# Optimization experiments

Hardware: AMD Instinct MI355X
Metric: run time of the kernel (lower is better)

## Reference

```python
import jax, jax.numpy as jnp
import numpy as np

EMBED_DIM = 512
NUM_HEADS = 8
HEAD_DIM = EMBED_DIM // NUM_HEADS
SHIFT_INIT = 5.0
EPS = 1e-6


def setup_inputs() -> dict:
    key = jax.random.key(0)
    ks = jax.random.split(key, 8)
    L, N, E = 2048, 4, EMBED_DIM
    query = jax.random.normal(ks[0], (L, N, E), dtype=jnp.float32)
    k_in = jax.random.normal(ks[1], (L, N, E), dtype=jnp.float32)
    v_in = jax.random.normal(ks[2], (L, N, E), dtype=jnp.float32)
    # MultiheadAttention packed projections
    in_proj_weight = jax.random.normal(ks[3], (3 * E, E), dtype=jnp.float32) / np.sqrt(E)
    in_proj_bias = jnp.zeros((3 * E,), dtype=jnp.float32)
    out_proj_weight = jax.random.normal(ks[4], (E, E), dtype=jnp.float32) / np.sqrt(E)
    out_proj_bias = jnp.zeros((E,), dtype=jnp.float32)
    # GeM parameters: p ~ N(1, 0.02), shift = 5
    p = 1.0 + 0.02 * jax.random.normal(ks[5], (E,), dtype=jnp.float32)
    shift = jnp.full((E,), SHIFT_INIT, dtype=jnp.float32)
    return {
        "query": query, "key": k_in, "value": v_in,
        "in_proj_weight": in_proj_weight, "in_proj_bias": in_proj_bias,
        "out_proj_weight": out_proj_weight, "out_proj_bias": out_proj_bias,
        "p": p, "shift": shift,
    }


def reference(query, key, value, in_proj_weight, in_proj_bias,
              out_proj_weight, out_proj_bias, p, shift):
    L, N, E = query.shape
    H, D = NUM_HEADS, HEAD_DIM
    w_q, w_k, w_v = jnp.split(in_proj_weight, 3, axis=0)   # each (E, E)
    b_q, b_k, b_v = jnp.split(in_proj_bias, 3, axis=0)

    def proj(x, w, b):
        # (L, N, E) -> (N, H, L, D)
        y = x @ w.T + b
        return y.reshape(L, N, H, D).transpose(1, 2, 0, 3)

    q = proj(query, w_q, b_q)
    k = proj(key, w_k, b_k)
    v = proj(value, w_v, b_v)

    scale = 1.0 / np.sqrt(D)
    scores = jnp.einsum('nhld,nhsd->nhls', q, k) * scale   # (N,H,L,S)
    attn = jax.nn.softmax(scores, axis=-1)

    # GeM pooling of values: shift -> power p -> weighted mean -> inverse power -> unshift
    p_h = p.reshape(H, D)[None, :, None, :]                # (1,H,1,D)
    shift_h = shift.reshape(H, D)[None, :, None, :]
    v_pos = jnp.maximum(v + shift_h, EPS)                  # keep base positive
    pooled = jnp.einsum('nhls,nhsd->nhld', attn, v_pos ** p_h)
    out_h = jnp.maximum(pooled, EPS) ** (1.0 / p_h) - shift_h  # (N,H,L,D)

    out = out_h.transpose(2, 0, 1, 3).reshape(L, N, E)     # back to (L,N,E)
    out = out @ out_proj_weight.T + out_proj_bias
    return out
```

## Files before the change

### kernel.cpp

```cpp
#include <hip/hip_runtime.h>
#include <hip/hip_bf16.h>

#define E_DIM 512
#define N_BATCH 4
#define L_SEQ 2048
#define N_HEADS 8
#define H_DIM 64
#define N_ROWS (L_SEQ * N_BATCH)
#define EPS_F 1e-6f
#define SC_Q 0.18033688f

typedef __attribute__((ext_vector_type(8))) short bf16x8;
typedef __attribute__((ext_vector_type(8))) _Float16 f16x8;
typedef __attribute__((ext_vector_type(4))) float f32x4;
typedef __attribute__((ext_vector_type(16))) float f32x16;

__device__ __forceinline__ void split2(float f, __hip_bfloat16& h, __hip_bfloat16& l) {
  h = __float2bfloat16(f);
  l = __float2bfloat16(f - __bfloat162float(h));
}

__device__ __forceinline__ unsigned int packf16(float a, float b) {
  union { _Float16 h[2]; unsigned int u; } c;
  c.h[0] = (_Float16)a;
  c.h[1] = (_Float16)b;
  return c.u;
}

__global__ __launch_bounds__(256) void wconv_kernel(
    const float* __restrict__ wio, const float* __restrict__ wo,
    __hip_bfloat16* __restrict__ wiohi, __hip_bfloat16* __restrict__ wiolo,
    __hip_bfloat16* __restrict__ wohi, __hip_bfloat16* __restrict__ wolo) {
  const int g = blockIdx.x * 256 + threadIdx.x;
  const float* src;
  __hip_bfloat16 *dh, *dl;
  int i;
  if (g < 196608) { src = wio; dh = wiohi; dl = wiolo; i = g * 4; }
  else            { src = wo;  dh = wohi;  dl = wolo;  i = (g - 196608) * 4; }
  const float4 f = *(const float4*)(src + i);
  alignas(8) __hip_bfloat16 h[4], l[4];
  split2(f.x, h[0], l[0]); split2(f.y, h[1], l[1]);
  split2(f.z, h[2], l[2]); split2(f.w, h[3], l[3]);
  *(uint2*)(dh + i) = *(const uint2*)h;
  *(uint2*)(dl + i) = *(const uint2*)l;
}

__global__ __launch_bounds__(256, 3) void proj_qkv_kernel(
    const float* __restrict__ xq, const float* __restrict__ xk,
    const float* __restrict__ xv, const __hip_bfloat16* __restrict__ whi,
    const float* __restrict__ bias, const float* __restrict__ pw,
    const float* __restrict__ sw,
    _Float16* __restrict__ qbuf, _Float16* __restrict__ kbuf,
    float* __restrict__ ubuf) {
  __shared__ __hip_bfloat16 Xh[128][40];
  __shared__ __hip_bfloat16 Xl[128][40];
  __shared__ __hip_bfloat16 Wh[128][40];
  const int z = blockIdx.z;
  const int row0 = blockIdx.x * 128;
  const int col0 = blockIdx.y * 128;
  const float* __restrict__ xsrc = (z == 0) ? xq : (z == 1) ? xk : xv;
  const int tid = threadIdx.x;
  const int lane = tid & 63;
  const int wv = tid >> 6;
  const int lidx = lane & 15;
  const int quad = lane >> 4;
  const int srow = tid >> 1;
  const int scol = (tid & 1) * 16;

  f32x4 acc[2][8];
#pragma unroll
  for (int rt = 0; rt < 2; ++rt)
#pragma unroll
    for (int ct = 0; ct < 8; ++ct) acc[rt][ct] = (f32x4){0.f, 0.f, 0.f, 0.f};

  const int ar0 = wv * 32 + lidx;

  for (int kt = 0; kt < 16; ++kt) {
    const int k0 = kt * 32;
    {
      const float* xp = xsrc + (size_t)(row0 + srow) * E_DIM + k0 + scol;
      float f[16];
      *(float4*)&f[0]  = ((const float4*)xp)[0];
      *(float4*)&f[4]  = ((const float4*)xp)[1];
      *(float4*)&f[8]  = ((const float4*)xp)[2];
      *(float4*)&f[12] = ((const float4*)xp)[3];
      alignas(16) __hip_bfloat16 hi[16], lo[16];
#pragma unroll
      for (int j = 0; j < 16; ++j) split2(f[j], hi[j], lo[j]);
      *(uint4*)&Xh[srow][scol]     = ((const uint4*)hi)[0];
      *(uint4*)&Xh[srow][scol + 8] = ((const uint4*)hi)[1];
      *(uint4*)&Xl[srow][scol]     = ((const uint4*)lo)[0];
      *(uint4*)&Xl[srow][scol + 8] = ((const uint4*)lo)[1];
    }
    {
      const size_t wof = (size_t)(z * E_DIM + col0 + srow) * E_DIM + k0 + scol;
      *(uint4*)&Wh[srow][scol]     = ((const uint4*)(whi + wof))[0];
      *(uint4*)&Wh[srow][scol + 8] = ((const uint4*)(whi + wof))[1];
    }
    __syncthreads();

    const bf16x8 ah0 = *(const bf16x8*)&Xh[ar0][quad * 8];
    const bf16x8 ah1 = *(const bf16x8*)&Xh[ar0 + 16][quad * 8];
    const bf16x8 al0 = *(const bf16x8*)&Xl[ar0][quad * 8];
    const bf16x8 al1 = *(const bf16x8*)&Xl[ar0 + 16][quad * 8];
#pragma unroll
    for (int ct = 0; ct < 8; ++ct) {
      const bf16x8 bh = *(const bf16x8*)&Wh[ct * 16 + lidx][quad * 8];
      acc[0][ct] = __builtin_amdgcn_mfma_f32_16x16x32_bf16(ah0, bh, acc[0][ct], 0, 0, 0);
      acc[0][ct] = __builtin_amdgcn_mfma_f32_16x16x32_bf16(al0, bh, acc[0][ct], 0, 0, 0);
      acc[1][ct] = __builtin_amdgcn_mfma_f32_16x16x32_bf16(ah1, bh, acc[1][ct], 0, 0, 0);
      acc[1][ct] = __builtin_amdgcn_mfma_f32_16x16x32_bf16(al1, bh, acc[1][ct], 0, 0, 0);
    }
    __syncthreads();
  }

  if (z < 2) {
    _Float16* __restrict__ dst = (z == 0) ? qbuf : kbuf;
    const float scale = (z == 0) ? SC_Q : 1.0f;
    float bv[8];
#pragma unroll
    for (int ct = 0; ct < 8; ++ct) bv[ct] = bias[z * E_DIM + col0 + ct * 16 + lidx];
#pragma unroll
    for (int rt = 0; rt < 2; ++rt)
#pragma unroll
      for (int ct = 0; ct < 8; ++ct) {
        const int e = col0 + ct * 16 + lidx;
        const int h = e >> 6, d = e & 63;
#pragma unroll
        for (int reg = 0; reg < 4; ++reg) {
          const int R = row0 + wv * 32 + rt * 16 + quad * 4 + reg;
          const int lpos = R >> 2, nb = R & 3;
          dst[(((size_t)nb * N_HEADS + h) * L_SEQ + lpos) * H_DIM + d] =
              (_Float16)((acc[rt][ct][reg] + bv[ct]) * scale);
        }
      }
  } else {
    float bv[8], pv[8], sv[8];
#pragma unroll
    for (int ct = 0; ct < 8; ++ct) {
      const int e = col0 + ct * 16 + lidx;
      bv[ct] = bias[2 * E_DIM + e]; pv[ct] = pw[e]; sv[ct] = sw[e];
    }
#pragma unroll
    for (int rt = 0; rt < 2; ++rt)
#pragma unroll
      for (int ct = 0; ct < 8; ++ct) {
        const int e = col0 + ct * 16 + lidx;
        const int h = e >> 6, d = e & 63;
#pragma unroll
        for (int reg = 0; reg < 4; ++reg) {
          const int R = row0 + wv * 32 + rt * 16 + quad * 4 + reg;
          const int lpos = R >> 2, nb = R & 3;
          const float y = acc[rt][ct][reg] + bv[ct];
          const float vp = fmaxf(y + sv[ct], EPS_F);
          ubuf[(((size_t)nb * N_HEADS + h) * L_SEQ + lpos) * H_DIM + d] =
              __powf(vp, pv[ct]);
        }
      }
  }
}

__global__ __launch_bounds__(256) void transp_kernel(
    const float* __restrict__ u, _Float16* __restrict__ uT) {
  __shared__ float T[64][65];
  const int lt = blockIdx.x, h = blockIdx.y, nb = blockIdx.z;
  const int tid = threadIdx.x;
  const int r = tid >> 2;
  const int cb = (tid & 3) * 16;
  const size_t srcbase = ((size_t)nb * N_HEADS + h) * L_SEQ + lt * 64;
  {
    const float* p = u + (srcbase + r) * H_DIM + cb;
    *(float4*)&T[r][cb + 0]  = ((const float4*)p)[0];
    *(float4*)&T[r][cb + 4]  = ((const float4*)p)[1];
    *(float4*)&T[r][cb + 8]  = ((const float4*)p)[2];
    *(float4*)&T[r][cb + 12] = ((const float4*)p)[3];
  }
  __syncthreads();
  alignas(16) _Float16 hv[16];
#pragma unroll
  for (int j = 0; j < 16; ++j) hv[j] = (_Float16)T[cb + j][r];
  const size_t dst = (((size_t)nb * N_HEADS + h) * H_DIM + r) * L_SEQ + lt * 64 + cb;
  *(uint4*)(uT + dst)     = ((const uint4*)hv)[0];
  *(uint4*)(uT + dst + 8) = ((const uint4*)hv)[1];
}

__global__ __launch_bounds__(128, 2) void attn_kernel(
    const _Float16* __restrict__ qbuf, const _Float16* __restrict__ kbuf,
    const _Float16* __restrict__ uT, const float* __restrict__ pw,
    const float* __restrict__ sw, __hip_bfloat16* __restrict__ ohhi,
    __hip_bfloat16* __restrict__ ohlo) {
  __shared__ _Float16 Ks[64][72];
  __shared__ _Float16 Us[64][72];
  const int qt = blockIdx.x, h = blockIdx.y, nb = blockIdx.z;
  const int q0 = qt * 128;
  const int tid = threadIdx.x;
  const int lane = tid & 63;
  const int wv = tid >> 6;
  const int lm = lane & 31;
  const int kg = lane >> 5;
  const int srow = tid >> 1;
  const int scb = (tid & 1) * 32;
  const size_t headbase = ((size_t)nb * N_HEADS + h) * L_SEQ;
  const size_t dbase = ((size_t)nb * N_HEADS + h) * H_DIM;

  f16x8 bq[2][4];
#pragma unroll
  for (int nt = 0; nt < 2; ++nt)
#pragma unroll
    for (int kc = 0; kc < 4; ++kc)
      bq[nt][kc] = *(const f16x8*)(qbuf +
          (headbase + q0 + wv * 64 + nt * 32 + lm) * H_DIM + kc * 16 + kg * 8);

  f32x16 o[2][2];
  o[0][0] = (f32x16)(0.f); o[0][1] = (f32x16)(0.f);
  o[1][0] = (f32x16)(0.f); o[1][1] = (f32x16)(0.f);
  float lsum[2] = {0.f, 0.f};

  for (int scn = 0; scn < 32; ++scn) {
    const int s0 = scn * 64;
    __syncthreads();
    {
      const _Float16* kp = kbuf + (headbase + s0 + srow) * H_DIM + scb;
      *(uint4*)&Ks[srow][scb + 0]  = ((const uint4*)kp)[0];
      *(uint4*)&Ks[srow][scb + 8]  = ((const uint4*)kp)[1];
      *(uint4*)&Ks[srow][scb + 16] = ((const uint4*)kp)[2];
      *(uint4*)&Ks[srow][scb + 24] = ((const uint4*)kp)[3];
      const _Float16* up = uT + (dbase + srow) * L_SEQ + s0 + scb;
      *(uint4*)&Us[srow][scb + 0]  = ((const uint4*)up)[0];
      *(uint4*)&Us[srow][scb + 8]  = ((const uint4*)up)[1];
      *(uint4*)&Us[srow][scb + 16] = ((const uint4*)up)[2];
      *(uint4*)&Us[srow][scb + 24] = ((const uint4*)up)[3];
    }
    __syncthreads();

    f32x16 sc[2][2];
    sc[0][0] = (f32x16)(0.f); sc[0][1] = (f32x16)(0.f);
    sc[1][0] = (f32x16)(0.f); sc[1][1] = (f32x16)(0.f);
#pragma unroll
    for (int kc = 0; kc < 4; ++kc) {
      const f16x8 ak0 = *(const f16x8*)&Ks[lm][kc * 16 + kg * 8];
      const f16x8 ak1 = *(const f16x8*)&Ks[32 + lm][kc * 16 + kg * 8];
      sc[0][0] = __builtin_amdgcn_mfma_f32_32x32x16_f16(ak0, bq[0][kc], sc[0][0], 0, 0, 0);
      sc[0][1] = __builtin_amdgcn_mfma_f32_32x32x16_f16(ak1, bq[0][kc], sc[0][1], 0, 0, 0);
      sc[1][0] = __builtin_amdgcn_mfma_f32_32x32x16_f16(ak0, bq[1][kc], sc[1][0], 0, 0, 0);
      sc[1][1] = __builtin_amdgcn_mfma_f32_32x32x16_f16(ak1, bq[1][kc], sc[1][1], 0, 0, 0);
    }

    unsigned int P2[2][2][4][2];
#pragma unroll
    for (int nt = 0; nt < 2; ++nt)
#pragma unroll
      for (int mt = 0; mt < 2; ++mt)
#pragma unroll
        for (int g = 0; g < 4; ++g) {
          const float p0 = __builtin_amdgcn_exp2f(sc[nt][mt][4 * g + 0]);
          const float p1 = __builtin_amdgcn_exp2f(sc[nt][mt][4 * g + 1]);
          const float p2 = __builtin_amdgcn_exp2f(sc[nt][mt][4 * g + 2]);
          const float p3 = __builtin_amdgcn_exp2f(sc[nt][mt][4 * g + 3]);
          lsum[nt] += (p0 + p1) + (p2 + p3);
          P2[nt][mt][g][0] = packf16(p0, p1);
          P2[nt][mt][g][1] = packf16(p2, p3);
        }

#pragma unroll
    for (int kc = 0; kc < 4; ++kc) {
      const int mt = kc >> 1;
      const f16x8 au0 = *(const f16x8*)&Us[lm][kc * 16 + kg * 8];
      const f16x8 au1 = *(const f16x8*)&Us[32 + lm][kc * 16 + kg * 8];
#pragma unroll
      for (int nt = 0; nt < 2; ++nt) {
        const int gx = (2 * kc) & 3, gy = (2 * kc + 1) & 3;
        const unsigned int x0 = P2[nt][mt][gx][0], x1 = P2[nt][mt][gx][1];
        const unsigned int y0 = P2[nt][mt][gy][0], y1 = P2[nt][mt][gy][1];
        const unsigned int sA = kg ? x0 : y0, sB = kg ? x1 : y1;
        const unsigned int rA = (unsigned int)__shfl_xor((int)sA, 32);
        const unsigned int rB = (unsigned int)__shfl_xor((int)sB, 32);
        union { unsigned int u[4]; f16x8 v; } bp;
        bp.u[0] = kg ? rA : x0;
        bp.u[1] = kg ? rB : x1;
        bp.u[2] = kg ? y0 : rA;
        bp.u[3] = kg ? y1 : rB;
        o[nt][0] = __builtin_amdgcn_mfma_f32_32x32x16_f16(au0, bp.v, o[nt][0], 0, 0, 0);
        o[nt][1] = __builtin_amdgcn_mfma_f32_32x32x16_f16(au1, bp.v, o[nt][1], 0, 0, 0);
      }
    }
  }

#pragma unroll
  for (int nt = 0; nt < 2; ++nt) {
    const float l = lsum[nt] + __shfl_xor(lsum[nt], 32);
    const float inv = 1.0f / l;
    const int qg = q0 + wv * 64 + nt * 32 + lm;
    const size_t base = ((size_t)qg * N_BATCH + nb) * E_DIM + h * H_DIM;
#pragma unroll
    for (int mt2 = 0; mt2 < 2; ++mt2)
#pragma unroll
      for (int g = 0; g < 4; ++g) {
        alignas(8) __hip_bfloat16 hb[4], lb[4];
#pragma unroll
        for (int i = 0; i < 4; ++i) {
          const int d = mt2 * 32 + 8 * g + 4 * kg + i;
          const int e = h * H_DIM + d;
          const float pooled = o[nt][mt2][4 * g + i] * inv;
          const float val = __powf(fmaxf(pooled, EPS_F), 1.0f / pw[e]) - sw[e];
          split2(val, hb[i], lb[i]);
        }
        const int d0 = mt2 * 32 + 8 * g + 4 * kg;
        *(uint2*)(ohhi + base + d0) = *(const uint2*)hb;
        *(uint2*)(ohlo + base + d0) = *(const uint2*)lb;
      }
  }
}

__global__ __launch_bounds__(256, 4) void out_proj_kernel(
    const __hip_bfloat16* __restrict__ xhi, const __hip_bfloat16* __restrict__ xlo,
    const __hip_bfloat16* __restrict__ whi, const __hip_bfloat16* __restrict__ wlo,
    const float* __restrict__ bias, float* __restrict__ out) {
  __shared__ __hip_bfloat16 Xh[128][40];
  __shared__ __hip_bfloat16 Xl[128][40];
  __shared__ __hip_bfloat16 Wh[64][40];
  __shared__ __hip_bfloat16 Wl[64][40];
  const int row0 = blockIdx.x * 128;
  const int col0 = blockIdx.y * 64;
  const int tid = threadIdx.x;
  const int lane = tid & 63;
  const int wv = tid >> 6;
  const int lidx = lane & 15;
  const int quad = lane >> 4;
  const int srow = tid >> 1;
  const int scol = (tid & 1) * 16;
  const int wrow = tid >> 2;
  const int wcol = (tid & 3) * 8;

  f32x4 acc[2][4];
#pragma unroll
  for (int rt = 0; rt < 2; ++rt)
#pragma unroll
    for (int ct = 0; ct < 4; ++ct) acc[rt][ct] = (f32x4){0.f, 0.f, 0.f, 0.f};

  const int ar0 = wv * 32 + lidx;

  for (int kt = 0; kt < 16; ++kt) {
    const int k0 = kt * 32;
    {
      const size_t xof = (size_t)(row0 + srow) * E_DIM + k0 + scol;
      *(uint4*)&Xh[srow][scol]     = ((const uint4*)(xhi + xof))[0];
      *(uint4*)&Xh[srow][scol + 8] = ((const uint4*)(xhi + xof))[1];
      *(uint4*)&Xl[srow][scol]     = ((const uint4*)(xlo + xof))[0];
      *(uint4*)&Xl[srow][scol + 8] = ((const uint4*)(xlo + xof))[1];
      const size_t wof = (size_t)(col0 + wrow) * E_DIM + k0 + wcol;
      *(uint4*)&Wh[wrow][wcol] = *(const uint4*)(whi + wof);
      *(uint4*)&Wl[wrow][wcol] = *(const uint4*)(wlo + wof);
    }
    __syncthreads();

    const bf16x8 ah0 = *(const bf16x8*)&Xh[ar0][quad * 8];
    const bf16x8 ah1 = *(const bf16x8*)&Xh[ar0 + 16][quad * 8];
    const bf16x8 al0 = *(const bf16x8*)&Xl[ar0][quad * 8];
    const bf16x8 al1 = *(const bf16x8*)&Xl[ar0 + 16][quad * 8];
#pragma unroll
    for (int ct = 0; ct < 4; ++ct) {
      const bf16x8 bh = *(const bf16x8*)&Wh[ct * 16 + lidx][quad * 8];
      const bf16x8 bl = *(const bf16x8*)&Wl[ct * 16 + lidx][quad * 8];
      acc[0][ct] = __builtin_amdgcn_mfma_f32_16x16x32_bf16(ah0, bh, acc[0][ct], 0, 0, 0);
      acc[0][ct] = __builtin_amdgcn_mfma_f32_16x16x32_bf16(al0, bh, acc[0][ct], 0, 0, 0);
      acc[0][ct] = __builtin_amdgcn_mfma_f32_16x16x32_bf16(ah0, bl, acc[0][ct], 0, 0, 0);
      acc[1][ct] = __builtin_amdgcn_mfma_f32_16x16x32_bf16(ah1, bh, acc[1][ct], 0, 0, 0);
      acc[1][ct] = __builtin_amdgcn_mfma_f32_16x16x32_bf16(al1, bh, acc[1][ct], 0, 0, 0);
      acc[1][ct] = __builtin_amdgcn_mfma_f32_16x16x32_bf16(ah1, bl, acc[1][ct], 0, 0, 0);
    }
    __syncthreads();
  }

  float bv[4];
#pragma unroll
  for (int ct = 0; ct < 4; ++ct) bv[ct] = bias[col0 + ct * 16 + lidx];
#pragma unroll
  for (int rt = 0; rt < 2; ++rt)
#pragma unroll
    for (int ct = 0; ct < 4; ++ct) {
      const int c = col0 + ct * 16 + lidx;
#pragma unroll
      for (int reg = 0; reg < 4; ++reg) {
        const int R = row0 + wv * 32 + rt * 16 + quad * 4 + reg;
        out[(size_t)R * E_DIM + c] = acc[rt][ct][reg] + bv[ct];
      }
    }
}

extern "C" void kernel_launch(void* const* d_in, const int* in_sizes, int n_in,
                              void* d_out, int out_size, void* d_ws, size_t ws_size,
                              hipStream_t stream) {
  const float* q_in = (const float*)d_in[0];
  const float* k_in = (const float*)d_in[1];
  const float* v_in = (const float*)d_in[2];
  const float* wio  = (const float*)d_in[3];
  const float* bio  = (const float*)d_in[4];
  const float* wo   = (const float*)d_in[5];
  const float* bo   = (const float*)d_in[6];
  const float* pw   = (const float*)d_in[7];
  const float* sw   = (const float*)d_in[8];

  const size_t NE = (size_t)N_ROWS * E_DIM;
  _Float16* qbuf = (_Float16*)d_ws;
  _Float16* kbuf = qbuf + NE;
  float* ubuf = (float*)(kbuf + NE);
  _Float16* uT = (_Float16*)(ubuf + NE);
  __hip_bfloat16* wiohi = (__hip_bfloat16*)(uT + NE);
  __hip_bfloat16* wiolo = wiohi + 786432;
  __hip_bfloat16* wohi  = wiolo + 786432;
  __hip_bfloat16* wolo  = wohi + 262144;
  __hip_bfloat16* ohhi = (__hip_bfloat16*)ubuf;
  __hip_bfloat16* ohlo = ohhi + NE;

  wconv_kernel<<<dim3(1024), 256, 0, stream>>>(wio, wo, wiohi, wiolo, wohi, wolo);
  proj_qkv_kernel<<<dim3(64, 4, 3), 256, 0, stream>>>(q_in, k_in, v_in, wiohi,
                                                      bio, pw, sw, qbuf, kbuf, ubuf);
  transp_kernel<<<dim3(32, 8, 4), 256, 0, stream>>>(ubuf, uT);
  attn_kernel<<<dim3(16, 8, 4), 128, 0, stream>>>(qbuf, kbuf, uT, pw, sw,
                                                  ohhi, ohlo);
  out_proj_kernel<<<dim3(64, 8), 256, 0, stream>>>(ohhi, ohlo, wohi, wolo,
                                                   bo, (float*)d_out);
}
```

Measured before the change: 288.7 us.

## Fuse value transpose into projection epilogue and drop LDS staging in attention

The value projection epilogue now writes the powered values directly as fp16 in the transposed (d, L) layout, which removes the separate transpose kernel and the fp32 intermediate buffer. The attention kernel becomes single-wave blocks of 32 queries that read K and the transposed values straight from global memory instead of staging them in shared memory with barriers. This saves a launch and a round trip of intermediate data, and gives four times as many attention blocks. In exchange, the transposed stores are strided 2-byte scatters, and K/V reuse now depends on cache hits rather than shared memory, with each K/V tile fetched by four times as many blocks.

```diff
diff --git a/kernel.cpp b/kernel.cpp
--- a/kernel.cpp
+++ b/kernel.cpp
@@ -51,7 +51,7 @@
     const float* __restrict__ bias, const float* __restrict__ pw,
     const float* __restrict__ sw,
     _Float16* __restrict__ qbuf, _Float16* __restrict__ kbuf,
-    float* __restrict__ ubuf) {
+    _Float16* __restrict__ uT) {
   __shared__ __hip_bfloat16 Xh[128][40];
   __shared__ __hip_bfloat16 Xl[128][40];
   __shared__ __hip_bfloat16 Wh[128][40];
@@ -141,175 +141,121 @@
       const int e = col0 + ct * 16 + lidx;
       bv[ct] = bias[2 * E_DIM + e]; pv[ct] = pw[e]; sv[ct] = sw[e];
     }
+    const int lposb = (row0 >> 2) + wv * 8;
 #pragma unroll
     for (int rt = 0; rt < 2; ++rt)
 #pragma unroll
       for (int ct = 0; ct < 8; ++ct) {
         const int e = col0 + ct * 16 + lidx;
         const int h = e >> 6, d = e & 63;
+        const int lpos = lposb + rt * 4 + quad;
 #pragma unroll
         for (int reg = 0; reg < 4; ++reg) {
-          const int R = row0 + wv * 32 + rt * 16 + quad * 4 + reg;
-          const int lpos = R >> 2, nb = R & 3;
           const float y = acc[rt][ct][reg] + bv[ct];
           const float vp = fmaxf(y + sv[ct], EPS_F);
-          ubuf[(((size_t)nb * N_HEADS + h) * L_SEQ + lpos) * H_DIM + d] =
-              __powf(vp, pv[ct]);
+          uT[(((size_t)reg * N_HEADS + h) * H_DIM + d) * L_SEQ + lpos] =
+              (_Float16)__powf(vp, pv[ct]);
         }
       }
   }
 }
 
-__global__ __launch_bounds__(256) void transp_kernel(
-    const float* __restrict__ u, _Float16* __restrict__ uT) {
-  __shared__ float T[64][65];
-  const int lt = blockIdx.x, h = blockIdx.y, nb = blockIdx.z;
-  const int tid = threadIdx.x;
-  const int r = tid >> 2;
-  const int cb = (tid & 3) * 16;
-  const size_t srcbase = ((size_t)nb * N_HEADS + h) * L_SEQ + lt * 64;
-  {
-    const float* p = u + (srcbase + r) * H_DIM + cb;
-    *(float4*)&T[r][cb + 0]  = ((const float4*)p)[0];
-    *(float4*)&T[r][cb + 4]  = ((const float4*)p)[1];
-    *(float4*)&T[r][cb + 8]  = ((const float4*)p)[2];
-    *(float4*)&T[r][cb + 12] = ((const float4*)p)[3];
-  }
-  __syncthreads();
-  alignas(16) _Float16 hv[16];
-#pragma unroll
-  for (int j = 0; j < 16; ++j) hv[j] = (_Float16)T[cb + j][r];
-  const size_t dst = (((size_t)nb * N_HEADS + h) * H_DIM + r) * L_SEQ + lt * 64 + cb;
-  *(uint4*)(uT + dst)     = ((const uint4*)hv)[0];
-  *(uint4*)(uT + dst + 8) = ((const uint4*)hv)[1];
-}
-
-__global__ __launch_bounds__(128, 2) void attn_kernel(
+__global__ __launch_bounds__(64, 2) void attn_kernel(
     const _Float16* __restrict__ qbuf, const _Float16* __restrict__ kbuf,
     const _Float16* __restrict__ uT, const float* __restrict__ pw,
     const float* __restrict__ sw, __hip_bfloat16* __restrict__ ohhi,
     __hip_bfloat16* __restrict__ ohlo) {
-  __shared__ _Float16 Ks[64][72];
-  __shared__ _Float16 Us[64][72];
   const int qt = blockIdx.x, h = blockIdx.y, nb = blockIdx.z;
-  const int q0 = qt * 128;
-  const int tid = threadIdx.x;
-  const int lane = tid & 63;
-  const int wv = tid >> 6;
+  const int q0 = qt * 32;
+  const int lane = threadIdx.x;
   const int lm = lane & 31;
   const int kg = lane >> 5;
-  const int srow = tid >> 1;
-  const int scb = (tid & 1) * 32;
   const size_t headbase = ((size_t)nb * N_HEADS + h) * L_SEQ;
   const size_t dbase = ((size_t)nb * N_HEADS + h) * H_DIM;
 
-  f16x8 bq[2][4];
-#pragma unroll
-  for (int nt = 0; nt < 2; ++nt)
-#pragma unroll
-    for (int kc = 0; kc < 4; ++kc)
-      bq[nt][kc] = *(const f16x8*)(qbuf +
-          (headbase + q0 + wv * 64 + nt * 32 + lm) * H_DIM + kc * 16 + kg * 8);
-
-  f32x16 o[2][2];
-  o[0][0] = (f32x16)(0.f); o[0][1] = (f32x16)(0.f);
-  o[1][0] = (f32x16)(0.f); o[1][1] = (f32x16)(0.f);
-  float lsum[2] = {0.f, 0.f};
+  f16x8 bq[4];
+#pragma unroll
+  for (int kc = 0; kc < 4; ++kc)
+    bq[kc] = *(const f16x8*)(qbuf + (headbase + q0 + lm) * H_DIM + kc * 16 + kg * 8);
+
+  f32x16 o[2];
+  o[0] = (f32x16)(0.f); o[1] = (f32x16)(0.f);
+  float lsum = 0.f;
 
   for (int scn = 0; scn < 32; ++scn) {
     const int s0 = scn * 64;
-    __syncthreads();
-    {
-      const _Float16* kp = kbuf + (headbase + s0 + srow) * H_DIM + scb;
-      *(uint4*)&Ks[srow][scb + 0]  = ((const uint4*)kp)[0];
-      *(uint4*)&Ks[srow][scb + 8]  = ((const uint4*)kp)[1];
-      *(uint4*)&Ks[srow][scb + 16] = ((const uint4*)kp)[2];
-      *(uint4*)&Ks[srow][scb + 24] = ((const uint4*)kp)[3];
-      const _Float16* up = uT + (dbase + srow) * L_SEQ + s0 + scb;
-      *(uint4*)&Us[srow][scb + 0]  = ((const uint4*)up)[0];
-      *(uint4*)&Us[srow][scb + 8]  = ((const uint4*)up)[1];
-      *(uint4*)&Us[srow][scb + 16] = ((const uint4*)up)[2];
-      *(uint4*)&Us[srow][scb + 24] = ((const uint4*)up)[3];
-    }
-    __syncthreads();
-
-    f32x16 sc[2][2];
-    sc[0][0] = (f32x16)(0.f); sc[0][1] = (f32x16)(0.f);
-    sc[1][0] = (f32x16)(0.f); sc[1][1] = (f32x16)(0.f);
+    const _Float16* k0p = kbuf + (headbase + s0 + lm) * H_DIM;
+    const _Float16* k1p = kbuf + (headbase + s0 + 32 + lm) * H_DIM;
+
+    f32x16 sc0 = (f32x16)(0.f), sc1 = (f32x16)(0.f);
 #pragma unroll
     for (int kc = 0; kc < 4; ++kc) {
-      const f16x8 ak0 = *(const f16x8*)&Ks[lm][kc * 16 + kg * 8];
-      const f16x8 ak1 = *(const f16x8*)&Ks[32 + lm][kc * 16 + kg * 8];
-      sc[0][0] = __builtin_amdgcn_mfma_f32_32x32x16_f16(ak0, bq[0][kc], sc[0][0], 0, 0, 0);
-      sc[0][1] = __builtin_amdgcn_mfma_f32_32x32x16_f16(ak1, bq[0][kc], sc[0][1], 0, 0, 0);
-      sc[1][0] = __builtin_amdgcn_mfma_f32_32x32x16_f16(ak0, bq[1][kc], sc[1][0], 0, 0, 0);
-      sc[1][1] = __builtin_amdgcn_mfma_f32_32x32x16_f16(ak1, bq[1][kc], sc[1][1], 0, 0, 0);
-    }
-
-    unsigned int P2[2][2][4][2];
-#pragma unroll
-    for (int nt = 0; nt < 2; ++nt)
-#pragma unroll
-      for (int mt = 0; mt < 2; ++mt)
-#pragma unroll
-        for (int g = 0; g < 4; ++g) {
-          const float p0 = __builtin_amdgcn_exp2f(sc[nt][mt][4 * g + 0]);
-          const float p1 = __builtin_amdgcn_exp2f(sc[nt][mt][4 * g + 1]);
-          const float p2 = __builtin_amdgcn_exp2f(sc[nt][mt][4 * g + 2]);
-          const float p3 = __builtin_amdgcn_exp2f(sc[nt][mt][4 * g + 3]);
-          lsum[nt] += (p0 + p1) + (p2 + p3);
-          P2[nt][mt][g][0] = packf16(p0, p1);
-          P2[nt][mt][g][1] = packf16(p2, p3);
-        }
-
+      const f16x8 ak0 = *(const f16x8*)(k0p + kc * 16 + kg * 8);
+      const f16x8 ak1 = *(const f16x8*)(k1p + kc * 16 + kg * 8);
+      sc0 = __builtin_amdgcn_mfma_f32_32x32x16_f16(ak0, bq[kc], sc0, 0, 0, 0);
+      sc1 = __builtin_amdgcn_mfma_f32_32x32x16_f16(ak1, bq[kc], sc1, 0, 0, 0);
+    }
+
+    unsigned int P2[2][4][2];
+#pragma unroll
+    for (int mt = 0; mt < 2; ++mt) {
+      const f32x16 s = mt ? sc1 : sc0;
+#pragma unroll
+      for (int g = 0; g < 4; ++g) {
+        const float p0 = __builtin_amdgcn_exp2f(s[4 * g + 0]);
+        const float p1 = __builtin_amdgcn_exp2f(s[4 * g + 1]);
+        const float p2 = __builtin_amdgcn_exp2f(s[4 * g + 2]);
+        const float p3 = __builtin_amdgcn_exp2f(s[4 * g + 3]);
+        lsum += (p0 + p1) + (p2 + p3);
+        P2[mt][g][0] = packf16(p0, p1);
+        P2[mt][g][1] = packf16(p2, p3);
+      }
+    }
+
+    const _Float16* u0p = uT + (dbase + lm) * L_SEQ + s0;
+    const _Float16* u1p = uT + (dbase + 32 + lm) * L_SEQ + s0;
 #pragma unroll
     for (int kc = 0; kc < 4; ++kc) {
       const int mt = kc >> 1;
-      const f16x8 au0 = *(const f16x8*)&Us[lm][kc * 16 + kg * 8];
-      const f16x8 au1 = *(const f16x8*)&Us[32 + lm][kc * 16 + kg * 8];
-#pragma unroll
-      for (int nt = 0; nt < 2; ++nt) {
-        const int gx = (2 * kc) & 3, gy = (2 * kc + 1) & 3;
-        const unsigned int x0 = P2[nt][mt][gx][0], x1 = P2[nt][mt][gx][1];
-        const unsigned int y0 = P2[nt][mt][gy][0], y1 = P2[nt][mt][gy][1];
-        const unsigned int sA = kg ? x0 : y0, sB = kg ? x1 : y1;
-        const unsigned int rA = (unsigned int)__shfl_xor((int)sA, 32);
-        const unsigned int rB = (unsigned int)__shfl_xor((int)sB, 32);
-        union { unsigned int u[4]; f16x8 v; } bp;
-        bp.u[0] = kg ? rA : x0;
-        bp.u[1] = kg ? rB : x1;
-        bp.u[2] = kg ? y0 : rA;
-        bp.u[3] = kg ? y1 : rB;
-        o[nt][0] = __builtin_amdgcn_mfma_f32_32x32x16_f16(au0, bp.v, o[nt][0], 0, 0, 0);
-        o[nt][1] = __builtin_amdgcn_mfma_f32_32x32x16_f16(au1, bp.v, o[nt][1], 0, 0, 0);
-      }
+      const f16x8 au0 = *(const f16x8*)(u0p + kc * 16 + kg * 8);
+      const f16x8 au1 = *(const f16x8*)(u1p + kc * 16 + kg * 8);
+      const int gx = (2 * kc) & 3, gy = (2 * kc + 1) & 3;
+      const unsigned int x0 = P2[mt][gx][0], x1 = P2[mt][gx][1];
+      const unsigned int y0 = P2[mt][gy][0], y1 = P2[mt][gy][1];
+      const unsigned int sA = kg ? x0 : y0, sB = kg ? x1 : y1;
+      const unsigned int rA = (unsigned int)__shfl_xor((int)sA, 32);
+      const unsigned int rB = (unsigned int)__shfl_xor((int)sB, 32);
+      union { unsigned int u[4]; f16x8 v; } bp;
+      bp.u[0] = kg ? rA : x0;
+      bp.u[1] = kg ? rB : x1;
+      bp.u[2] = kg ? y0 : rA;
+      bp.u[3] = kg ? y1 : rB;
+      o[0] = __builtin_amdgcn_mfma_f32_32x32x16_f16(au0, bp.v, o[0], 0, 0, 0);
+      o[1] = __builtin_amdgcn_mfma_f32_32x32x16_f16(au1, bp.v, o[1], 0, 0, 0);
     }
   }
 
-#pragma unroll
-  for (int nt = 0; nt < 2; ++nt) {
-    const float l = lsum[nt] + __shfl_xor(lsum[nt], 32);
-    const float inv = 1.0f / l;
-    const int qg = q0 + wv * 64 + nt * 32 + lm;
-    const size_t base = ((size_t)qg * N_BATCH + nb) * E_DIM + h * H_DIM;
-#pragma unroll
-    for (int mt2 = 0; mt2 < 2; ++mt2)
-#pragma unroll
-      for (int g = 0; g < 4; ++g) {
-        alignas(8) __hip_bfloat16 hb[4], lb[4];
-#pragma unroll
-        for (int i = 0; i < 4; ++i) {
-          const int d = mt2 * 32 + 8 * g + 4 * kg + i;
-          const int e = h * H_DIM + d;
-          const float pooled = o[nt][mt2][4 * g + i] * inv;
-          const float val = __powf(fmaxf(pooled, EPS_F), 1.0f / pw[e]) - sw[e];
-          split2(val, hb[i], lb[i]);
-        }
-        const int d0 = mt2 * 32 + 8 * g + 4 * kg;
-        *(uint2*)(ohhi + base + d0) = *(const uint2*)hb;
-        *(uint2*)(ohlo + base + d0) = *(const uint2*)lb;
-      }
-  }
+  const float l = lsum + __shfl_xor(lsum, 32);
+  const float inv = 1.0f / l;
+  const int qg = q0 + lm;
+  const size_t base = ((size_t)qg * N_BATCH + nb) * E_DIM + h * H_DIM;
+#pragma unroll
+  for (int mt2 = 0; mt2 < 2; ++mt2)
+#pragma unroll
+    for (int g = 0; g < 4; ++g) {
+      alignas(8) __hip_bfloat16 hb[4], lb[4];
+#pragma unroll
+      for (int i = 0; i < 4; ++i) {
+        const int d = mt2 * 32 + 8 * g + 4 * kg + i;
+        const int e = h * H_DIM + d;
+        const float pooled = o[mt2][4 * g + i] * inv;
+        const float val = __powf(fmaxf(pooled, EPS_F), 1.0f / pw[e]) - sw[e];
+        split2(val, hb[i], lb[i]);
+      }
+      const int d0 = mt2 * 32 + 8 * g + 4 * kg;
+      *(uint2*)(ohhi + base + d0) = *(const uint2*)hb;
+      *(uint2*)(ohlo + base + d0) = *(const uint2*)lb;
+    }
 }
 
 __global__ __launch_bounds__(256, 4) void out_proj_kernel(
@@ -404,21 +350,19 @@
   const size_t NE = (size_t)N_ROWS * E_DIM;
   _Float16* qbuf = (_Float16*)d_ws;
   _Float16* kbuf = qbuf + NE;
-  float* ubuf = (float*)(kbuf + NE);
-  _Float16* uT = (_Float16*)(ubuf + NE);
+  __hip_bfloat16* ohhi = (__hip_bfloat16*)(kbuf + NE);
+  __hip_bfloat16* ohlo = ohhi + NE;
+  _Float16* uT = (_Float16*)(ohlo + NE);
   __hip_bfloat16* wiohi = (__hip_bfloat16*)(uT + NE);
   __hip_bfloat16* wiolo = wiohi + 786432;
   __hip_bfloat16* wohi  = wiolo + 786432;
   __hip_bfloat16* wolo  = wohi + 262144;
-  __hip_bfloat16* ohhi = (__hip_bfloat16*)ubuf;
-  __hip_bfloat16* ohlo = ohhi + NE;
 
   wconv_kernel<<<dim3(1024), 256, 0, stream>>>(wio, wo, wiohi, wiolo, wohi, wolo);
   proj_qkv_kernel<<<dim3(64, 4, 3), 256, 0, stream>>>(q_in, k_in, v_in, wiohi,
-                                                      bio, pw, sw, qbuf, kbuf, ubuf);
-  transp_kernel<<<dim3(32, 8, 4), 256, 0, stream>>>(ubuf, uT);
-  attn_kernel<<<dim3(16, 8, 4), 128, 0, stream>>>(qbuf, kbuf, uT, pw, sw,
-                                                  ohhi, ohlo);
+                                                      bio, pw, sw, qbuf, kbuf, uT);
+  attn_kernel<<<dim3(64, 8, 4), 64, 0, stream>>>(qbuf, kbuf, uT, pw, sw,
+                                                 ohhi, ohlo);
   out_proj_kernel<<<dim3(64, 8), 256, 0, stream>>>(ohhi, ohlo, wohi, wolo,
                                                    bo, (float*)d_out);
 }
```

Measured after the change: 319.8 us. 1.11x slower.
